# Kernel optimization log

Hardware: AMD Instinct MI355X
Metric: run time of the kernel (lower is better)

## Reference

```python
import jax, jax.numpy as jnp
import numpy as np

N, T, D, H = 32, 1024, 1152, 16
DH = D // H            # 72
MLP = int(D * 4.0)     # 4608
EPS = 1e-6


def setup_inputs() -> dict:
    key = jax.random.key(0)
    ks = jax.random.split(key, 14)
    s = 0.02
    return {
        "x": jax.random.normal(ks[0], (N, T, D), jnp.float32),
        "c": jax.random.normal(ks[1], (N, D), jnp.float32),
        "qkv_w": jax.random.normal(ks[2], (D, 3 * D), jnp.float32) * s,
        "qkv_b": jax.random.normal(ks[3], (3 * D,), jnp.float32) * s,
        "proj_w": jax.random.normal(ks[4], (D, D), jnp.float32) * s,
        "proj_b": jax.random.normal(ks[5], (D,), jnp.float32) * s,
        "fc1_w": jax.random.normal(ks[6], (D, MLP), jnp.float32) * s,
        "fc1_b": jax.random.normal(ks[7], (MLP,), jnp.float32) * s,
        "fc2_w": jax.random.normal(ks[8], (MLP, D), jnp.float32) * s,
        "fc2_b": jax.random.normal(ks[9], (D,), jnp.float32) * s,
        "ada_w": jax.random.normal(ks[10], (D, 6 * D), jnp.float32) * s,
        "ada_b": jax.random.normal(ks[11], (6 * D,), jnp.float32) * s,
    }


def _layernorm(x):
    m = jnp.mean(x, axis=-1, keepdims=True)
    v = jnp.var(x, axis=-1, keepdims=True)
    return (x - m) * jax.lax.rsqrt(v + EPS)


def _modulate(x, shift, scale):
    # shift, scale: (N, D) broadcast over T
    return x * (1.0 + scale[:, None, :]) + shift[:, None, :]


def _attention(x, qkv_w, qkv_b, proj_w, proj_b):
    n, t, d = x.shape
    scale = DH ** (-0.5)
    qkv = x @ qkv_w + qkv_b                       # (N,T,3D)
    qkv = qkv.reshape(n, t, 3, H, DH)
    q, k, v = qkv[:, :, 0], qkv[:, :, 1], qkv[:, :, 2]  # each (N,T,H,DH)
    # Faithful to source: matmul over the LAST two dims -> per-token
    # head-vs-head attention of shape (N,T,H,H), softmax over heads.
    attn = jnp.einsum("nthd,ntkd->nthk", q * scale, k)
    attn = jax.nn.softmax(attn, axis=-1)
    out = jnp.einsum("nthk,ntkd->nthd", attn, v)  # (N,T,H,DH)
    out = out.transpose(0, 2, 1, 3).reshape(n, t, d)  # faithful scramble
    return out @ proj_w + proj_b


def _mlp(x, fc1_w, fc1_b, fc2_w, fc2_b):
    h = jax.nn.gelu(x @ fc1_w + fc1_b, approximate=False)  # exact GELU (torch default)
    return h @ fc2_w + fc2_b


def reference(x, c, qkv_w, qkv_b, proj_w, proj_b, fc1_w, fc1_b, fc2_w, fc2_b,
              ada_w, ada_b):
    ada = jax.nn.silu(c) @ ada_w + ada_b          # (N, 6D)
    (shift_msa, scale_msa, gate_msa,
     shift_mlp, scale_mlp, gate_mlp) = jnp.split(ada, 6, axis=1)
    x = x + gate_msa[:, None, :] * _attention(
        _modulate(_layernorm(x), shift_msa, scale_msa),
        qkv_w, qkv_b, proj_w, proj_b)
    x = x + gate_mlp[:, None, :] * _mlp(
        _modulate(_layernorm(x), shift_mlp, scale_mlp),
        fc1_w, fc1_b, fc2_w, fc2_b)
    return x
```

## Files before the change

### kernel.cpp

```cpp
#include <hip/hip_runtime.h>

#define DEV __device__ __forceinline__

typedef __attribute__((ext_vector_type(8))) short short8;
typedef __attribute__((ext_vector_type(8))) __bf16 bf16x8;
typedef __attribute__((ext_vector_type(4))) float f32x4;

#define TD      1024
#define DD      1152
#define DHH     72
#define MLPD    4608
#define QKVN    3456
#define ADAN    6912
#define MROWS   32768

DEV unsigned short f32_to_bf16(float f) {
  unsigned int u = __float_as_uint(f);
  u += 0x7fffu + ((u >> 16) & 1u);
  return (unsigned short)(u >> 16);
}

DEV void gl16(const void* g, void* l) {
  __builtin_amdgcn_global_load_lds((__attribute__((address_space(1))) void*)g,
                                   (__attribute__((address_space(3))) void*)l,
                                   16, 0, 0);
}

DEV bf16x8 zero_bf16x8() {
  short8 z = {0, 0, 0, 0, 0, 0, 0, 0};
  return __builtin_bit_cast(bf16x8, z);
}

DEV float gelu_exact(float v) {
  return 0.5f * v * (1.0f + erff(v * 0.70710678118654752f));
}

#define WAITV(n) asm volatile("s_waitcnt vmcnt(" #n ")" ::: "memory")

__global__ __launch_bounds__(256) void wtrans_kernel(const float* __restrict__ W,
                                                     unsigned short* __restrict__ Wt,
                                                     int K, int N) {
  __shared__ unsigned short tile[32][33];
  const int nb = blockIdx.x * 32, kb = blockIdx.y * 32;
  const int tx = threadIdx.x, ty = threadIdx.y;
  #pragma unroll
  for (int i = ty; i < 32; i += 8)
    tile[i][tx] = f32_to_bf16(W[(size_t)(kb + i) * N + nb + tx]);
  __syncthreads();
  #pragma unroll
  for (int i = ty; i < 32; i += 8)
    Wt[(size_t)(nb + i) * K + kb + tx] = tile[tx][i];
}

__global__ __launch_bounds__(256) void ada_kernel(const float* __restrict__ c,
                                                  const float* __restrict__ ada_w,
                                                  const float* __restrict__ ada_b,
                                                  float* __restrict__ ada_out) {
  __shared__ float sc[DD];
  const int n = blockIdx.y;
  const int col = blockIdx.x * 256 + threadIdx.x;
  for (int i = threadIdx.x; i < DD; i += 256) {
    float v = c[(size_t)n * DD + i];
    sc[i] = v / (1.0f + __expf(-v));
  }
  __syncthreads();
  float acc = ada_b[col];
  #pragma unroll 8
  for (int k = 0; k < DD; ++k)
    acc += sc[k] * ada_w[(size_t)k * ADAN + col];
  ada_out[(size_t)n * ADAN + col] = acc;
}

__global__ __launch_bounds__(256) void ln_mod_kernel(const float* __restrict__ X,
                                                     const float* __restrict__ ada,
                                                     int soff,
                                                     unsigned short* __restrict__ out) {
  const int row = blockIdx.x;
  const int batch = row >> 10;
  const float* xr = X + (size_t)row * DD;
  const int t = threadIdx.x;

  float4 v0 = reinterpret_cast<const float4*>(xr)[t];
  float4 v1 = make_float4(0.f, 0.f, 0.f, 0.f);
  const bool has2 = (t < 32);
  if (has2) v1 = reinterpret_cast<const float4*>(xr)[256 + t];

  float s  = v0.x + v0.y + v0.z + v0.w + v1.x + v1.y + v1.z + v1.w;
  float sq = v0.x*v0.x + v0.y*v0.y + v0.z*v0.z + v0.w*v0.w
           + v1.x*v1.x + v1.y*v1.y + v1.z*v1.z + v1.w*v1.w;
  #pragma unroll
  for (int m = 1; m < 64; m <<= 1) {
    s  += __shfl_xor(s, m);
    sq += __shfl_xor(sq, m);
  }
  __shared__ float red[8];
  const int wv = t >> 6;
  if ((t & 63) == 0) { red[wv] = s; red[4 + wv] = sq; }
  __syncthreads();
  s  = red[0] + red[1] + red[2] + red[3];
  sq = red[4] + red[5] + red[6] + red[7];
  const float mean = s * (1.0f / 1152.0f);
  const float var  = sq * (1.0f / 1152.0f) - mean * mean;
  const float rstd = rsqrtf(var + 1e-6f);

  const float* shp = ada + (size_t)batch * ADAN + soff;
  const float* scp = shp + DD;
  unsigned short* orow = out + (size_t)row * DD;

  {
    const int col = t * 4;
    ushort4 o4;
    o4.x = f32_to_bf16((v0.x - mean) * rstd * (1.0f + scp[col + 0]) + shp[col + 0]);
    o4.y = f32_to_bf16((v0.y - mean) * rstd * (1.0f + scp[col + 1]) + shp[col + 1]);
    o4.z = f32_to_bf16((v0.z - mean) * rstd * (1.0f + scp[col + 2]) + shp[col + 2]);
    o4.w = f32_to_bf16((v0.w - mean) * rstd * (1.0f + scp[col + 3]) + shp[col + 3]);
    reinterpret_cast<ushort4*>(orow)[t] = o4;
  }
  if (has2) {
    const int col = 1024 + t * 4;
    ushort4 o4;
    o4.x = f32_to_bf16((v1.x - mean) * rstd * (1.0f + scp[col + 0]) + shp[col + 0]);
    o4.y = f32_to_bf16((v1.y - mean) * rstd * (1.0f + scp[col + 1]) + shp[col + 1]);
    o4.z = f32_to_bf16((v1.z - mean) * rstd * (1.0f + scp[col + 2]) + shp[col + 2]);
    o4.w = f32_to_bf16((v1.w - mean) * rstd * (1.0f + scp[col + 3]) + shp[col + 3]);
    reinterpret_cast<ushort4*>(orow)[256 + t] = o4;
  }
}

template <int EPI>
__global__ __launch_bounds__(512) void gemm8p(
    const unsigned short* __restrict__ A, const unsigned short* __restrict__ Bt,
    const float* __restrict__ bias, const float* __restrict__ ada, int ada_off,
    const float* __restrict__ resid, unsigned short* __restrict__ out_bf,
    float* __restrict__ out_f, int N, int K, int ntn) {
  __shared__ unsigned short lds[65536];
  const int tid = threadIdx.x;
  const int lane = tid & 63, w = tid >> 6;
  const int wm = w >> 2, wn = w & 3;
  const int l15 = lane & 15, lg = lane >> 4;

  const int nwg = 128 * ntn, cpx = nwg >> 3;
  const int wg = (blockIdx.x & 7) * cpx + (blockIdx.x >> 3);
  const int bm = wg / ntn, bn = wg - bm * ntn;

  const unsigned short* __restrict__ Ag = A + (size_t)bm * 256 * K;
  const unsigned short* __restrict__ Bg = Bt + (size_t)bn * 256 * K;

  const int rp0 = tid >> 3;
  const int ch0 = (tid & 7) ^ (rp0 & 7);

#define STGU(P, RS, LB, BUFB, KT) do {                                                   \
    gl16((P) + (size_t)((RS) + rp0) * K + (size_t)(KT) * 64 + ch0 * 8,                   \
         &lds[(BUFB) + (LB) + tid * 8]);                                                 \
    gl16((P) + (size_t)((RS) + rp0 + 64) * K + (size_t)(KT) * 64 + ch0 * 8,              \
         &lds[(BUFB) + (LB) + 4096 + tid * 8]);                                          \
  } while (0)

  const int chA0 = (lg ^ (l15 & 7)) * 8;
  const int chA1 = chA0 ^ 32;
  const int arow0 = wm * 64 + l15;
  const int brow0 = wn * 32 + l15;

  f32x4 acc[2][2][4][2];
  #pragma unroll
  for (int a = 0; a < 2; ++a)
    #pragma unroll
    for (int b = 0; b < 2; ++b)
      #pragma unroll
      for (int m = 0; m < 4; ++m)
        #pragma unroll
        for (int n2 = 0; n2 < 2; ++n2)
          acc[a][b][m][n2] = (f32x4){0.f, 0.f, 0.f, 0.f};

#define LDA(DST, MQ)                                                                     \
  _Pragma("unroll") for (int mf = 0; mf < 4; ++mf) {                                     \
    DST[mf][0] = *(const bf16x8*)&lb[(arow0 + (MQ)*128 + mf*16) * 64 + chA0];            \
    DST[mf][1] = *(const bf16x8*)&lb[(arow0 + (MQ)*128 + mf*16) * 64 + chA1];            \
  }
#define LDB(DST, NQ)                                                                     \
  _Pragma("unroll") for (int nf = 0; nf < 2; ++nf) {                                     \
    DST[nf][0] = *(const bf16x8*)&lb[16384 + (brow0 + (NQ)*128 + nf*16) * 64 + chA0];    \
    DST[nf][1] = *(const bf16x8*)&lb[16384 + (brow0 + (NQ)*128 + nf*16) * 64 + chA1];    \
  }
#define QMFMA(MQ, NQ, AA, BB)                                                            \
  do {                                                                                   \
    __builtin_amdgcn_s_setprio(1);                                                       \
    _Pragma("unroll") for (int mf = 0; mf < 4; ++mf)                                     \
      _Pragma("unroll") for (int nf = 0; nf < 2; ++nf) {                                 \
        acc[MQ][NQ][mf][nf] = __builtin_amdgcn_mfma_f32_16x16x32_bf16(                   \
            AA[mf][0], BB[nf][0], acc[MQ][NQ][mf][nf], 0, 0, 0);                         \
        acc[MQ][NQ][mf][nf] = __builtin_amdgcn_mfma_f32_16x16x32_bf16(                   \
            AA[mf][1], BB[nf][1], acc[MQ][NQ][mf][nf], 0, 0, 0);                         \
      }                                                                                  \
    __builtin_amdgcn_s_setprio(0);                                                       \
  } while (0)

  const int NT = K >> 6;

  STGU(Ag, 0, 0, 0, 0);
  STGU(Bg, 0, 16384, 0, 0);
  STGU(Bg, 128, 24576, 0, 0);
  STGU(Ag, 128, 8192, 0, 0);
  WAITV(4);
  __builtin_amdgcn_s_barrier();

  for (int t = 0; t < NT - 1; ++t) {
    const int cb = (t & 1) << 15, nb = cb ^ 32768;
    const unsigned short* lb = lds + cb;
    bf16x8 a0[4][2], a1[4][2], b0[2][2], b1[2][2];
    LDA(a0, 0) LDB(b0, 0)
    STGU(Ag, 0, 0, nb, t + 1);
    WAITV(4);
    __builtin_amdgcn_s_barrier();
    QMFMA(0, 0, a0, b0);
    LDB(b1, 1)
    STGU(Bg, 0, 16384, nb, t + 1);
    WAITV(4);
    __builtin_amdgcn_s_barrier();
    QMFMA(0, 1, a0, b1);
    LDA(a1, 1)
    STGU(Bg, 128, 24576, nb, t + 1);
    QMFMA(1, 1, a1, b1);
    STGU(Ag, 128, 8192, nb, t + 1);
    WAITV(4);
    __builtin_amdgcn_s_barrier();
    QMFMA(1, 0, a1, b0);
  }
  {
    const int cb = ((NT - 1) & 1) << 15;
    const unsigned short* lb = lds + cb;
    bf16x8 a0[4][2], a1[4][2], b0[2][2], b1[2][2];
    LDA(a0, 0) LDB(b0, 0)
    WAITV(2);
    __builtin_amdgcn_s_barrier();
    QMFMA(0, 0, a0, b0);
    LDB(b1, 1)
    WAITV(0);
    __builtin_amdgcn_s_barrier();
    QMFMA(0, 1, a0, b1);
    LDA(a1, 1)
    QMFMA(1, 1, a1, b1);
    QMFMA(1, 0, a1, b0);
  }
#undef STGU
#undef LDA
#undef LDB
#undef QMFMA

  const int batch = bm >> 2;
  #pragma unroll
  for (int nq = 0; nq < 2; ++nq) {
    const int colbase = bn * 256 + nq * 128 + wn * 32;
    if (colbase >= N) continue;
    #pragma unroll
    for (int nf = 0; nf < 2; ++nf) {
      const int colg = colbase + nf * 16 + l15;
      const float bv = bias[colg];
      float g2 = 0.0f;
      if constexpr (EPI == 1 || EPI == 3) g2 = ada[(size_t)batch * ADAN + ada_off + colg];
      #pragma unroll
      for (int mq = 0; mq < 2; ++mq) {
        #pragma unroll
        for (int mf = 0; mf < 4; ++mf) {
          #pragma unroll
          for (int r = 0; r < 4; ++r) {
            const size_t row = (size_t)bm * 256 + wm * 64 + mq * 128 + mf * 16 + lg * 4 + r;
            const size_t idx = row * (size_t)N + colg;
            const float v = acc[mq][nq][mf][nf][r] + bv;
            if constexpr (EPI == 0)      out_bf[idx] = f32_to_bf16(v);
            else if constexpr (EPI == 2) out_bf[idx] = f32_to_bf16(gelu_exact(v));
            else if constexpr (EPI == 1) out_f[idx] = resid[idx] + g2 * v;
            else                         out_f[idx] = out_f[idx] + g2 * v;
          }
        }
      }
    }
  }
}

__global__ __launch_bounds__(256) void attn_kernel(const unsigned short* __restrict__ qkv,
                                                   unsigned short* __restrict__ y) {
  const int tid = threadIdx.x, w = tid >> 6, lane = tid & 63;
  const int l15 = lane & 15, lg = lane >> 4;
  const int tok = blockIdx.x * 4 + w;
  const int n = tok >> 10, t = tok & 1023;

  __shared__ unsigned short Pl[4][16 * 32];
  __shared__ unsigned short Vl[4][16 * 80];

  for (int i = lane; i < 16 * 32; i += 64)
    if ((i & 31) >= 16) Pl[w][i] = 0;

  const size_t rowb = (size_t)tok * QKVN;
  const float scale = 0.11785113019775793f;

  bf16x8 aq[3];
  #pragma unroll
  for (int kk = 0; kk < 3; ++kk) {
    const int d0 = kk * 32 + lg * 8;
    aq[kk] = (d0 < DHH) ? *(const bf16x8*)&qkv[rowb + l15 * DHH + d0] : zero_bf16x8();
  }

  for (int c = lane; c < 144; c += 64) {
    const int r = c / 9, cc = (c % 9) * 8;
    *(short8*)&Vl[w][r * 80 + cc] = *(const short8*)&qkv[rowb + 2 * DD + r * DHH + cc];
  }

  f32x4 s = (f32x4){0.f, 0.f, 0.f, 0.f};
  #pragma unroll
  for (int kk = 0; kk < 3; ++kk) {
    const int d0 = kk * 32 + lg * 8;
    bf16x8 bk = (d0 < DHH) ? *(const bf16x8*)&qkv[rowb + DD + l15 * DHH + d0] : zero_bf16x8();
    s = __builtin_amdgcn_mfma_f32_16x16x32_bf16(aq[kk], bk, s, 0, 0, 0);
  }

  float p[4], mx[4], ssum[4];
  #pragma unroll
  for (int r = 0; r < 4; ++r) { p[r] = s[r] * scale; mx[r] = p[r]; }
  #pragma unroll
  for (int mk = 1; mk <= 8; mk <<= 1)
    #pragma unroll
    for (int r = 0; r < 4; ++r) mx[r] = fmaxf(mx[r], __shfl_xor(mx[r], mk));
  #pragma unroll
  for (int r = 0; r < 4; ++r) { p[r] = __expf(p[r] - mx[r]); ssum[r] = p[r]; }
  #pragma unroll
  for (int mk = 1; mk <= 8; mk <<= 1)
    #pragma unroll
    for (int r = 0; r < 4; ++r) ssum[r] += __shfl_xor(ssum[r], mk);

  #pragma unroll
  for (int r = 0; r < 4; ++r)
    Pl[w][(lg * 4 + r) * 32 + l15] = f32_to_bf16(p[r] / ssum[r]);

  bf16x8 pa = *(const bf16x8*)&Pl[w][l15 * 32 + lg * 8];
  const int kb = (lg & 1) * 8;
  f32x4 o[5];
  #pragma unroll
  for (int df = 0; df < 5; ++df) {
    short8 bvv;
    #pragma unroll
    for (int j = 0; j < 8; ++j)
      bvv[j] = (short)Vl[w][(kb + j) * 80 + df * 16 + l15];
    o[df] = __builtin_amdgcn_mfma_f32_16x16x32_bf16(
        pa, __builtin_bit_cast(bf16x8, bvv), (f32x4){0.f, 0.f, 0.f, 0.f}, 0, 0, 0);
  }

  unsigned short* yb = y + (size_t)n * (TD * DD);
  #pragma unroll
  for (int df = 0; df < 5; ++df) {
    const int d = df * 16 + l15;
    if (d < DHH) {
      #pragma unroll
      for (int r = 0; r < 4; ++r) {
        const int h = lg * 4 + r;
        yb[h * 73728 + t * DHH + d] = f32_to_bf16(o[df][r]);
      }
    }
  }
}

extern "C" void kernel_launch(void* const* d_in, const int* in_sizes, int n_in,
                              void* d_out, int out_size, void* d_ws, size_t ws_size,
                              hipStream_t stream) {
  (void)in_sizes; (void)n_in; (void)out_size; (void)ws_size;
  const float* x      = (const float*)d_in[0];
  const float* c      = (const float*)d_in[1];
  const float* qkv_w  = (const float*)d_in[2];
  const float* qkv_b  = (const float*)d_in[3];
  const float* proj_w = (const float*)d_in[4];
  const float* proj_b = (const float*)d_in[5];
  const float* fc1_w  = (const float*)d_in[6];
  const float* fc1_b  = (const float*)d_in[7];
  const float* fc2_w  = (const float*)d_in[8];
  const float* fc2_b  = (const float*)d_in[9];
  const float* ada_w  = (const float*)d_in[10];
  const float* ada_b  = (const float*)d_in[11];
  float* out = (float*)d_out;

  char* ws = (char*)d_ws;
  unsigned short* hbuf    = (unsigned short*)ws;
  unsigned short* qkvbuf  = hbuf;
  unsigned short* attnbuf = hbuf + (size_t)MROWS * QKVN;
  size_t off = 301989888ull;
  unsigned short* xm    = (unsigned short*)(ws + off); off += 75497472ull;
  unsigned short* wtq   = (unsigned short*)(ws + off); off += (size_t)3584 * DD * 2;
  unsigned short* wtp   = (unsigned short*)(ws + off); off += (size_t)1280 * DD * 2;
  unsigned short* wtf1  = (unsigned short*)(ws + off); off += (size_t)4608 * DD * 2;
  unsigned short* wtf2  = (unsigned short*)(ws + off); off += (size_t)1280 * MLPD * 2;
  float*          adab  = (float*)(ws + off); off += 884736ull;

  const dim3 tb(32, 8);
  hipLaunchKernelGGL(wtrans_kernel, dim3(QKVN / 32, DD / 32), tb, 0, stream, qkv_w, wtq, DD, QKVN);
  hipLaunchKernelGGL(wtrans_kernel, dim3(DD / 32, DD / 32),   tb, 0, stream, proj_w, wtp, DD, DD);
  hipLaunchKernelGGL(wtrans_kernel, dim3(MLPD / 32, DD / 32), tb, 0, stream, fc1_w, wtf1, DD, MLPD);
  hipLaunchKernelGGL(wtrans_kernel, dim3(DD / 32, MLPD / 32), tb, 0, stream, fc2_w, wtf2, MLPD, DD);

  hipLaunchKernelGGL(ada_kernel, dim3(ADAN / 256, 32), dim3(256), 0, stream, c, ada_w, ada_b, adab);

  hipLaunchKernelGGL(ln_mod_kernel, dim3(MROWS), dim3(256), 0, stream, x, adab, 0, xm);

  hipLaunchKernelGGL((gemm8p<0>), dim3(128 * 14), dim3(512), 0, stream,
                     xm, wtq, qkv_b, nullptr, 0, nullptr, qkvbuf, nullptr, QKVN, DD, 14);

  hipLaunchKernelGGL(attn_kernel, dim3(MROWS / 4), dim3(256), 0, stream, qkvbuf, attnbuf);

  hipLaunchKernelGGL((gemm8p<1>), dim3(128 * 5), dim3(512), 0, stream,
                     attnbuf, wtp, proj_b, adab, 2304, x, nullptr, out, DD, DD, 5);

  hipLaunchKernelGGL(ln_mod_kernel, dim3(MROWS), dim3(256), 0, stream, out, adab, 3456, xm);

  hipLaunchKernelGGL((gemm8p<2>), dim3(128 * 18), dim3(512), 0, stream,
                     xm, wtf1, fc1_b, nullptr, 0, nullptr, hbuf, nullptr, MLPD, DD, 18);

  hipLaunchKernelGGL((gemm8p<3>), dim3(128 * 5), dim3(512), 0, stream,
                     hbuf, wtf2, fc2_b, adab, 5760, nullptr, nullptr, out, DD, MLPD, 5);
}
```

Measured before the change: 1.770 ms.

## Prefetch next tile's low A/B fragments into ping-pong registers in GEMM loop

Restructures the GEMM main loop so the first-quadrant A and B fragments of the next K tile are read from LDS into registers at the end of the current tile. Two register sets alternate, and the loop is unrolled by two. The goal is to hide LDS read latency ahead of the first MFMA group of each tile, and to move the high-quadrant LDS reads to right after each barrier. In exchange it uses more VGPRs, which may lower occupancy or cause spills. The loop structure also assumes the tile count along K is even.

Result: slower. 2.862 ms (+61.7%).

```diff
diff --git a/kernel.cpp b/kernel.cpp
--- a/kernel.cpp
+++ b/kernel.cpp
@@ -172,15 +172,15 @@
         for (int n2 = 0; n2 < 2; ++n2)
           acc[a][b][m][n2] = (f32x4){0.f, 0.f, 0.f, 0.f};
 
-#define LDA(DST, MQ)                                                                     \
+#define LDA_FROM(PTR, DST, MQ)                                                           \
   _Pragma("unroll") for (int mf = 0; mf < 4; ++mf) {                                     \
-    DST[mf][0] = *(const bf16x8*)&lb[(arow0 + (MQ)*128 + mf*16) * 64 + chA0];            \
-    DST[mf][1] = *(const bf16x8*)&lb[(arow0 + (MQ)*128 + mf*16) * 64 + chA1];            \
-  }
-#define LDB(DST, NQ)                                                                     \
+    DST[mf][0] = *(const bf16x8*)&(PTR)[(arow0 + (MQ)*128 + mf*16) * 64 + chA0];         \
+    DST[mf][1] = *(const bf16x8*)&(PTR)[(arow0 + (MQ)*128 + mf*16) * 64 + chA1];         \
+  }
+#define LDB_FROM(PTR, DST, NQ)                                                           \
   _Pragma("unroll") for (int nf = 0; nf < 2; ++nf) {                                     \
-    DST[nf][0] = *(const bf16x8*)&lb[16384 + (brow0 + (NQ)*128 + nf*16) * 64 + chA0];    \
-    DST[nf][1] = *(const bf16x8*)&lb[16384 + (brow0 + (NQ)*128 + nf*16) * 64 + chA1];    \
+    DST[nf][0] = *(const bf16x8*)&(PTR)[16384 + (brow0 + (NQ)*128 + nf*16) * 64 + chA0]; \
+    DST[nf][1] = *(const bf16x8*)&(PTR)[16384 + (brow0 + (NQ)*128 + nf*16) * 64 + chA1]; \
   }
 #define QMFMA(MQ, NQ, AA, BB)                                                            \
   do {                                                                                   \
@@ -195,7 +195,38 @@
     __builtin_amdgcn_s_setprio(0);                                                       \
   } while (0)
 
+#define TILEBODY(T, ALO, BLO, ALO_N, BLO_N)                                              \
+  do {                                                                                   \
+    const int cb_ = ((T) & 1) << 15, nb_ = cb_ ^ 32768;                                  \
+    const unsigned short* lb_ = lds + cb_;                                               \
+    const unsigned short* lbn_ = lds + nb_;                                              \
+                                                                                \
+    STGU(Ag, 0, 0, nb_, (T) + 1);                                                        \
+    WAITV(4);                                                                            \
+    __builtin_amdgcn_s_barrier();                                                        \
+    LDB_FROM(lb_, bhi, 1)                                                                \
+    QMFMA(0, 0, ALO, BLO);                                                               \
+                                                                                \
+    STGU(Bg, 0, 16384, nb_, (T) + 1);                                                    \
+    WAITV(4);                                                                            \
+    __builtin_amdgcn_s_barrier();                                                        \
+    LDA_FROM(lb_, ahi, 1)                                                                \
+    QMFMA(0, 1, ALO, bhi);                                                               \
+                                                                       \
+    STGU(Bg, 128, 24576, nb_, (T) + 1);                                                  \
+    QMFMA(1, 1, ahi, bhi);                                                               \
+                                                                                \
+    STGU(Ag, 128, 8192, nb_, (T) + 1);                                                   \
+    WAITV(4);                                                                            \
+    __builtin_amdgcn_s_barrier();                                                        \
+    LDA_FROM(lbn_, ALO_N, 0)                                                             \
+    LDB_FROM(lbn_, BLO_N, 0)                                                             \
+    QMFMA(1, 0, ahi, BLO);                                                               \
+  } while (0)
+
   const int NT = K >> 6;
+
+  bf16x8 aloA[4][2], bloA[2][2], aloB[4][2], bloB[2][2], ahi[4][2], bhi[2][2];
 
   STGU(Ag, 0, 0, 0, 0);
   STGU(Bg, 0, 16384, 0, 0);
@@ -203,49 +234,33 @@
   STGU(Ag, 128, 8192, 0, 0);
   WAITV(4);
   __builtin_amdgcn_s_barrier();
-
-  for (int t = 0; t < NT - 1; ++t) {
-    const int cb = (t & 1) << 15, nb = cb ^ 32768;
-    const unsigned short* lb = lds + cb;
-    bf16x8 a0[4][2], a1[4][2], b0[2][2], b1[2][2];
-    LDA(a0, 0) LDB(b0, 0)
-    STGU(Ag, 0, 0, nb, t + 1);
-    WAITV(4);
-    __builtin_amdgcn_s_barrier();
-    QMFMA(0, 0, a0, b0);
-    LDB(b1, 1)
-    STGU(Bg, 0, 16384, nb, t + 1);
-    WAITV(4);
-    __builtin_amdgcn_s_barrier();
-    QMFMA(0, 1, a0, b1);
-    LDA(a1, 1)
-    STGU(Bg, 128, 24576, nb, t + 1);
-    QMFMA(1, 1, a1, b1);
-    STGU(Ag, 128, 8192, nb, t + 1);
-    WAITV(4);
-    __builtin_amdgcn_s_barrier();
-    QMFMA(1, 0, a1, b0);
-  }
+  LDA_FROM(lds, aloA, 0)
+  LDB_FROM(lds, bloA, 0)
+
+  for (int t = 0; t < NT - 2; t += 2) {
+    TILEBODY(t,     aloA, bloA, aloB, bloB);
+    TILEBODY(t + 1, aloB, bloB, aloA, bloA);
+  }
+  TILEBODY(NT - 2, aloA, bloA, aloB, bloB);
   {
-    const int cb = ((NT - 1) & 1) << 15;
-    const unsigned short* lb = lds + cb;
-    bf16x8 a0[4][2], a1[4][2], b0[2][2], b1[2][2];
-    LDA(a0, 0) LDB(b0, 0)
+    const int cb_ = ((NT - 1) & 1) << 15;
+    const unsigned short* lb_ = lds + cb_;
     WAITV(2);
     __builtin_amdgcn_s_barrier();
-    QMFMA(0, 0, a0, b0);
-    LDB(b1, 1)
+    LDB_FROM(lb_, bhi, 1)
+    QMFMA(0, 0, aloB, bloB);
     WAITV(0);
     __builtin_amdgcn_s_barrier();
-    QMFMA(0, 1, a0, b1);
-    LDA(a1, 1)
-    QMFMA(1, 1, a1, b1);
-    QMFMA(1, 0, a1, b0);
+    LDA_FROM(lb_, ahi, 1)
+    QMFMA(0, 1, aloB, bhi);
+    QMFMA(1, 1, ahi, bhi);
+    QMFMA(1, 0, ahi, bloB);
   }
 #undef STGU
-#undef LDA
-#undef LDB
+#undef LDA_FROM
+#undef LDB_FROM
 #undef QMFMA
+#undef TILEBODY
 
   const int batch = bm >> 2;
   #pragma unroll
```

## Pre-swizzle weights into MFMA fragment layout and load B directly to registers

Applied to the files above, without the earlier changes.

The weight transpose kernel now writes bf16 weights in a per-16-column, per-32-k fragment order that matches the MFMA B operand layout. The GEMM loads B fragments straight from global memory into registers, double-buffered across k-tiles, and stages only A through LDS, which halves LDS use and simplifies the loop into four sub-phases per tile with one barrier. The aim is to cut LDS traffic and barriers on the B side, which allows more occupancy. In exchange, B reads now go through global/L2 per wave, duplicated across the wm waves, and register pressure goes up from the two B sets.

New measurement: 2.001 ms. +13.1%, slower.

```diff
diff --git a/kernel.cpp b/kernel.cpp
--- a/kernel.cpp
+++ b/kernel.cpp
@@ -37,19 +37,20 @@
 
 #define WAITV(n) asm volatile("s_waitcnt vmcnt(" #n ")" ::: "memory")
 
-__global__ __launch_bounds__(256) void wtrans_kernel(const float* __restrict__ W,
-                                                     unsigned short* __restrict__ Wt,
-                                                     int K, int N) {
-  __shared__ unsigned short tile[32][33];
+__global__ __launch_bounds__(256) void wtrans_frag(const float* __restrict__ W,
+                                                   unsigned short* __restrict__ Bp,
+                                                   int K, int N) {
   const int nb = blockIdx.x * 32, kb = blockIdx.y * 32;
   const int tx = threadIdx.x, ty = threadIdx.y;
-  #pragma unroll
-  for (int i = ty; i < 32; i += 8)
-    tile[i][tx] = f32_to_bf16(W[(size_t)(kb + i) * N + nb + tx]);
-  __syncthreads();
-  #pragma unroll
-  for (int i = ty; i < 32; i += 8)
-    Wt[(size_t)(nb + i) * K + kb + tx] = tile[tx][i];
+  const size_t K16 = (size_t)K << 4;
+  #pragma unroll
+  for (int i = 0; i < 4; ++i) {
+    const int k = kb + ty + i * 8;
+    const int n = nb + tx;
+    const unsigned short v = f32_to_bf16(W[(size_t)k * N + n]);
+    Bp[(size_t)(n >> 4) * K16 + (size_t)(k >> 5) * 512 +
+       (size_t)(((n & 15) + ((k >> 3) & 3) * 16) * 8 + (k & 7))] = v;
+  }
 }
 
 __global__ __launch_bounds__(256) void ada_kernel(const float* __restrict__ c,
@@ -128,12 +129,12 @@
 }
 
 template <int EPI>
-__global__ __launch_bounds__(512) void gemm8p(
-    const unsigned short* __restrict__ A, const unsigned short* __restrict__ Bt,
+__global__ __launch_bounds__(512) void gemmB(
+    const unsigned short* __restrict__ A, const unsigned short* __restrict__ Bp,
     const float* __restrict__ bias, const float* __restrict__ ada, int ada_off,
     const float* __restrict__ resid, unsigned short* __restrict__ out_bf,
     float* __restrict__ out_f, int N, int K, int ntn) {
-  __shared__ unsigned short lds[65536];
+  __shared__ unsigned short lds[32768];
   const int tid = threadIdx.x;
   const int lane = tid & 63, w = tid >> 6;
   const int wm = w >> 2, wn = w & 3;
@@ -144,22 +145,33 @@
   const int bm = wg / ntn, bn = wg - bm * ntn;
 
   const unsigned short* __restrict__ Ag = A + (size_t)bm * 256 * K;
-  const unsigned short* __restrict__ Bg = Bt + (size_t)bn * 256 * K;
+  const size_t K16 = (size_t)K << 4;
+  const unsigned short* __restrict__ Bgl = Bp + (size_t)(bn * 16 + wn * 2) * K16 + lane * 8;
 
   const int rp0 = tid >> 3;
-  const int ch0 = (tid & 7) ^ (rp0 & 7);
-
-#define STGU(P, RS, LB, BUFB, KT) do {                                                   \
-    gl16((P) + (size_t)((RS) + rp0) * K + (size_t)(KT) * 64 + ch0 * 8,                   \
-         &lds[(BUFB) + (LB) + tid * 8]);                                                 \
-    gl16((P) + (size_t)((RS) + rp0 + 64) * K + (size_t)(KT) * 64 + ch0 * 8,              \
-         &lds[(BUFB) + (LB) + 4096 + tid * 8]);                                          \
+  const int ch0 = ((tid & 7) ^ (rp0 & 7)) * 8;
+
+#define STG_A(BUFS, KT) do {                                                              \
+    gl16(Ag + (size_t)(rp0) * K + (size_t)(KT) * 64 + ch0, &lds[(BUFS) + tid * 8]);       \
+    gl16(Ag + (size_t)(rp0 + 64) * K + (size_t)(KT) * 64 + ch0,                           \
+         &lds[(BUFS) + 4096 + tid * 8]);                                                  \
+    gl16(Ag + (size_t)(rp0 + 128) * K + (size_t)(KT) * 64 + ch0,                          \
+         &lds[(BUFS) + 8192 + tid * 8]);                                                  \
+    gl16(Ag + (size_t)(rp0 + 192) * K + (size_t)(KT) * 64 + ch0,                          \
+         &lds[(BUFS) + 12288 + tid * 8]);                                                 \
+  } while (0)
+
+#define LOAD_B(DST, KT) do {                                                              \
+    _Pragma("unroll") for (int nq_ = 0; nq_ < 2; ++nq_)                                   \
+      _Pragma("unroll") for (int nf_ = 0; nf_ < 2; ++nf_)                                 \
+        _Pragma("unroll") for (int kb_ = 0; kb_ < 2; ++kb_)                               \
+          DST[nq_][nf_][kb_] = *(const bf16x8*)&Bgl[(size_t)(nq_ * 8 + nf_) * K16 +       \
+                                                    ((KT) * 2 + kb_) * 512];              \
   } while (0)
 
   const int chA0 = (lg ^ (l15 & 7)) * 8;
   const int chA1 = chA0 ^ 32;
   const int arow0 = wm * 64 + l15;
-  const int brow0 = wn * 32 + l15;
 
   f32x4 acc[2][2][4][2];
   #pragma unroll
@@ -172,80 +184,57 @@
         for (int n2 = 0; n2 < 2; ++n2)
           acc[a][b][m][n2] = (f32x4){0.f, 0.f, 0.f, 0.f};
 
-#define LDA(DST, MQ)                                                                     \
-  _Pragma("unroll") for (int mf = 0; mf < 4; ++mf) {                                     \
-    DST[mf][0] = *(const bf16x8*)&lb[(arow0 + (MQ)*128 + mf*16) * 64 + chA0];            \
-    DST[mf][1] = *(const bf16x8*)&lb[(arow0 + (MQ)*128 + mf*16) * 64 + chA1];            \
-  }
-#define LDB(DST, NQ)                                                                     \
-  _Pragma("unroll") for (int nf = 0; nf < 2; ++nf) {                                     \
-    DST[nf][0] = *(const bf16x8*)&lb[16384 + (brow0 + (NQ)*128 + nf*16) * 64 + chA0];    \
-    DST[nf][1] = *(const bf16x8*)&lb[16384 + (brow0 + (NQ)*128 + nf*16) * 64 + chA1];    \
-  }
-#define QMFMA(MQ, NQ, AA, BB)                                                            \
-  do {                                                                                   \
-    __builtin_amdgcn_s_setprio(1);                                                       \
-    _Pragma("unroll") for (int mf = 0; mf < 4; ++mf)                                     \
-      _Pragma("unroll") for (int nf = 0; nf < 2; ++nf) {                                 \
-        acc[MQ][NQ][mf][nf] = __builtin_amdgcn_mfma_f32_16x16x32_bf16(                   \
-            AA[mf][0], BB[nf][0], acc[MQ][NQ][mf][nf], 0, 0, 0);                         \
-        acc[MQ][NQ][mf][nf] = __builtin_amdgcn_mfma_f32_16x16x32_bf16(                   \
-            AA[mf][1], BB[nf][1], acc[MQ][NQ][mf][nf], 0, 0, 0);                         \
-      }                                                                                  \
-    __builtin_amdgcn_s_setprio(0);                                                       \
+#define SUBPH(MQ, KB, BSET) do {                                                          \
+    bf16x8 af_[4];                                                                        \
+    _Pragma("unroll") for (int mf_ = 0; mf_ < 4; ++mf_)                                   \
+      af_[mf_] = *(const bf16x8*)&lb[(arow0 + (MQ) * 128 + mf_ * 16) * 64 +               \
+                                     ((KB) ? chA1 : chA0)];                               \
+    __builtin_amdgcn_s_setprio(1);                                                        \
+    _Pragma("unroll") for (int mf_ = 0; mf_ < 4; ++mf_)                                   \
+      _Pragma("unroll") for (int nq_ = 0; nq_ < 2; ++nq_)                                 \
+        _Pragma("unroll") for (int nf_ = 0; nf_ < 2; ++nf_)                               \
+          acc[MQ][nq_][mf_][nf_] = __builtin_amdgcn_mfma_f32_16x16x32_bf16(               \
+              af_[mf_], BSET[nq_][nf_][KB], acc[MQ][nq_][mf_][nf_], 0, 0, 0);             \
+    __builtin_amdgcn_s_setprio(0);                                                        \
   } while (0)
 
+#define TILE(T, BCUR, BNXT) do {                                                          \
+    const unsigned short* lb = lds + (((T) & 1) << 14);                                   \
+    STG_A((((T) + 1) & 1) << 14, (T) + 1);                                                \
+    LOAD_B(BNXT, (T) + 1);                                                                \
+    SUBPH(0, 0, BCUR);                                                                    \
+    SUBPH(0, 1, BCUR);                                                                    \
+    SUBPH(1, 0, BCUR);                                                                    \
+    SUBPH(1, 1, BCUR);                                                                    \
+    WAITV(0);                                                                             \
+    __builtin_amdgcn_s_barrier();                                                         \
+  } while (0)
+
   const int NT = K >> 6;
 
-  STGU(Ag, 0, 0, 0, 0);
-  STGU(Bg, 0, 16384, 0, 0);
-  STGU(Bg, 128, 24576, 0, 0);
-  STGU(Ag, 128, 8192, 0, 0);
-  WAITV(4);
+  bf16x8 BX[2][2][2], BY[2][2][2];
+
+  STG_A(0, 0);
+  LOAD_B(BX, 0);
+  WAITV(0);
   __builtin_amdgcn_s_barrier();
 
-  for (int t = 0; t < NT - 1; ++t) {
-    const int cb = (t & 1) << 15, nb = cb ^ 32768;
-    const unsigned short* lb = lds + cb;
-    bf16x8 a0[4][2], a1[4][2], b0[2][2], b1[2][2];
-    LDA(a0, 0) LDB(b0, 0)
-    STGU(Ag, 0, 0, nb, t + 1);
-    WAITV(4);
-    __builtin_amdgcn_s_barrier();
-    QMFMA(0, 0, a0, b0);
-    LDB(b1, 1)
-    STGU(Bg, 0, 16384, nb, t + 1);
-    WAITV(4);
-    __builtin_amdgcn_s_barrier();
-    QMFMA(0, 1, a0, b1);
-    LDA(a1, 1)
-    STGU(Bg, 128, 24576, nb, t + 1);
-    QMFMA(1, 1, a1, b1);
-    STGU(Ag, 128, 8192, nb, t + 1);
-    WAITV(4);
-    __builtin_amdgcn_s_barrier();
-    QMFMA(1, 0, a1, b0);
-  }
+  for (int t = 0; t < NT - 2; t += 2) {
+    TILE(t, BX, BY);
+    TILE(t + 1, BY, BX);
+  }
+  TILE(NT - 2, BX, BY);
   {
-    const int cb = ((NT - 1) & 1) << 15;
-    const unsigned short* lb = lds + cb;
-    bf16x8 a0[4][2], a1[4][2], b0[2][2], b1[2][2];
-    LDA(a0, 0) LDB(b0, 0)
-    WAITV(2);
-    __builtin_amdgcn_s_barrier();
-    QMFMA(0, 0, a0, b0);
-    LDB(b1, 1)
-    WAITV(0);
-    __builtin_amdgcn_s_barrier();
-    QMFMA(0, 1, a0, b1);
-    LDA(a1, 1)
-    QMFMA(1, 1, a1, b1);
-    QMFMA(1, 0, a1, b0);
-  }
-#undef STGU
-#undef LDA
-#undef LDB
-#undef QMFMA
+    const unsigned short* lb = lds + (((NT - 1) & 1) << 14);
+    SUBPH(0, 0, BY);
+    SUBPH(0, 1, BY);
+    SUBPH(1, 0, BY);
+    SUBPH(1, 1, BY);
+  }
+#undef STG_A
+#undef LOAD_B
+#undef SUBPH
+#undef TILE
 
   const int batch = bm >> 2;
   #pragma unroll
@@ -390,28 +379,28 @@
   float*          adab  = (float*)(ws + off); off += 884736ull;
 
   const dim3 tb(32, 8);
-  hipLaunchKernelGGL(wtrans_kernel, dim3(QKVN / 32, DD / 32), tb, 0, stream, qkv_w, wtq, DD, QKVN);
-  hipLaunchKernelGGL(wtrans_kernel, dim3(DD / 32, DD / 32),   tb, 0, stream, proj_w, wtp, DD, DD);
-  hipLaunchKernelGGL(wtrans_kernel, dim3(MLPD / 32, DD / 32), tb, 0, stream, fc1_w, wtf1, DD, MLPD);
-  hipLaunchKernelGGL(wtrans_kernel, dim3(DD / 32, MLPD / 32), tb, 0, stream, fc2_w, wtf2, MLPD, DD);
+  hipLaunchKernelGGL(wtrans_frag, dim3(QKVN / 32, DD / 32), tb, 0, stream, qkv_w, wtq, DD, QKVN);
+  hipLaunchKernelGGL(wtrans_frag, dim3(DD / 32, DD / 32),   tb, 0, stream, proj_w, wtp, DD, DD);
+  hipLaunchKernelGGL(wtrans_frag, dim3(MLPD / 32, DD / 32), tb, 0, stream, fc1_w, wtf1, DD, MLPD);
+  hipLaunchKernelGGL(wtrans_frag, dim3(DD / 32, MLPD / 32), tb, 0, stream, fc2_w, wtf2, MLPD, DD);
 
   hipLaunchKernelGGL(ada_kernel, dim3(ADAN / 256, 32), dim3(256), 0, stream, c, ada_w, ada_b, adab);
 
   hipLaunchKernelGGL(ln_mod_kernel, dim3(MROWS), dim3(256), 0, stream, x, adab, 0, xm);
 
-  hipLaunchKernelGGL((gemm8p<0>), dim3(128 * 14), dim3(512), 0, stream,
+  hipLaunchKernelGGL((gemmB<0>), dim3(128 * 14), dim3(512), 0, stream,
                      xm, wtq, qkv_b, nullptr, 0, nullptr, qkvbuf, nullptr, QKVN, DD, 14);
 
   hipLaunchKernelGGL(attn_kernel, dim3(MROWS / 4), dim3(256), 0, stream, qkvbuf, attnbuf);
 
-  hipLaunchKernelGGL((gemm8p<1>), dim3(128 * 5), dim3(512), 0, stream,
+  hipLaunchKernelGGL((gemmB<1>), dim3(128 * 5), dim3(512), 0, stream,
                      attnbuf, wtp, proj_b, adab, 2304, x, nullptr, out, DD, DD, 5);
 
   hipLaunchKernelGGL(ln_mod_kernel, dim3(MROWS), dim3(256), 0, stream, out, adab, 3456, xm);
 
-  hipLaunchKernelGGL((gemm8p<2>), dim3(128 * 18), dim3(512), 0, stream,
+  hipLaunchKernelGGL((gemmB<2>), dim3(128 * 18), dim3(512), 0, stream,
                      xm, wtf1, fc1_b, nullptr, 0, nullptr, hbuf, nullptr, MLPD, DD, 18);
 
-  hipLaunchKernelGGL((gemm8p<3>), dim3(128 * 5), dim3(512), 0, stream,
+  hipLaunchKernelGGL((gemmB<3>), dim3(128 * 5), dim3(512), 0, stream,
                      hbuf, wtf2, fc2_b, adab, 5760, nullptr, nullptr, out, DD, MLPD, 5);
 }
```
